# Kernel tuning notes

Measured on AMD Instinct MI355X. Metric: run time of the kernel, lower is better.

Reference implementation:

```python
import jax, jax.numpy as jnp
import numpy as np

WIDTH = 128


def setup_inputs() -> dict:
    key = jax.random.key(0)
    k_logits, k_w1, k_b1, k_w2, k_b2 = jax.random.split(key, 5)
    B, T, V = 32, 256, 4096
    logits = jax.random.normal(k_logits, (B, T, V), dtype=jnp.float32)
    # Linear(1, width): weight [width, 1] -> stored transposed as [1, width]
    w1 = jax.random.normal(k_w1, (1, WIDTH), dtype=jnp.float32) / jnp.sqrt(1.0)
    b1 = jax.random.normal(k_b1, (WIDTH,), dtype=jnp.float32) * 0.1
    # Linear(width, 1): weight [1, width] -> stored transposed as [width, 1]
    w2 = jax.random.normal(k_w2, (WIDTH, 1), dtype=jnp.float32) / jnp.sqrt(WIDTH)
    b2 = jax.random.normal(k_b2, (1,), dtype=jnp.float32) * 0.1
    return {"logits": logits, "w1": w1, "b1": b1, "w2": w2, "b2": b2}


def reference(logits, w1, b1, w2, b2):
    B, T, V = logits.shape
    logits_trim = logits[:, :-1, :]                       # [B, T-1, V]
    # entropy of softmax over the class dim; logits - logsumexp == log_softmax
    logp = jax.nn.log_softmax(logits_trim, axis=-1)       # [B, T-1, V]
    p = jnp.exp(logp)
    entropy = -jnp.sum(p * logp, axis=-1, keepdims=True)  # [B, T-1, 1]
    entropy_max = jnp.log(jnp.asarray(T, dtype=logits.dtype))  # log(num_steps)
    norm = 2.0 * entropy / entropy_max - 1.0              # [B, T-1, 1]
    # tiny 1 -> width -> 1 MLP
    hidden = jax.nn.relu(norm @ w1 + b1)                  # [B, T-1, width]
    lin = (2.0 * hidden) @ w2 + b2                        # [B, T-1, 1]
    # ns = [T-1, T-2, ..., 1]
    ns = jnp.arange(T - 1, 0, -1, dtype=logits.dtype).reshape(1, T - 1, 1)
    flags_trim = jax.nn.sigmoid(lin - jnp.log(ns))        # [B, T-1, 1]
    zeros = jnp.zeros((B, 1, 1), dtype=logits.dtype)
    ones = jnp.ones((B, 1, 1), dtype=logits.dtype)
    flags = jnp.concatenate([zeros, flags_trim, ones], axis=1)  # [B, T+1, 1]
    probabilities = jax.nn.softmax(logits, axis=2)        # [B, T, V]
    residuals = jnp.cumprod(1.0 - flags[:, :-1], axis=1)  # [B, T, 1] survival
    frequencies = probabilities * flags[:, 1:] * residuals  # [B, T, V]
    return frequencies
```

## Files before the change

### kernel.cpp

```cpp
#include <hip/hip_runtime.h>
#include <math.h>

#define T_DIM 256
#define V_DIM 4096
#define WIDTH 128

__device__ __forceinline__ float wave_max(float v) {
#pragma unroll
  for (int o = 32; o > 0; o >>= 1) v = fmaxf(v, __shfl_xor(v, o));
  return v;
}

__device__ __forceinline__ double wave_sum(double v) {
#pragma unroll
  for (int o = 32; o > 0; o >>= 1) v += __shfl_xor(v, o);
  return v;
}

__global__ __launch_bounds__(256) void row_stats(
    const float* __restrict__ logits,
    const float* __restrict__ w1, const float* __restrict__ b1,
    const float* __restrict__ w2, const float* __restrict__ b2,
    float* __restrict__ row_max, double* __restrict__ row_Z,
    double* __restrict__ row_flag) {
  const int row = blockIdx.x;
  const int t = row & (T_DIM - 1);
  const int tid = threadIdx.x;
  const int lane = tid & 63;
  const int wave = tid >> 6;

  const float4* src = (const float4*)(logits + (size_t)row * V_DIM);
  float4 xv[4];
#pragma unroll
  for (int k = 0; k < 4; ++k) xv[k] = src[tid + k * 256];

  float m = -INFINITY;
#pragma unroll
  for (int k = 0; k < 4; ++k)
    m = fmaxf(m, fmaxf(fmaxf(xv[k].x, xv[k].y), fmaxf(xv[k].z, xv[k].w)));
  m = wave_max(m);

  __shared__ float smax[4];
  __shared__ double szs[4], sss[4];
  if (lane == 0) smax[wave] = m;
  __syncthreads();
  m = fmaxf(fmaxf(smax[0], smax[1]), fmaxf(smax[2], smax[3]));

  double z = 0.0, s = 0.0;
#pragma unroll
  for (int k = 0; k < 4; ++k) {
    float vals[4] = {xv[k].x, xv[k].y, xv[k].z, xv[k].w};
#pragma unroll
    for (int j = 0; j < 4; ++j) {
      float sv = vals[j] - m;
      float ev = expf(sv);
      z += (double)ev;
      s += (double)ev * (double)sv;
    }
  }
  z = wave_sum(z);
  s = wave_sum(s);
  if (lane == 0) { szs[wave] = z; sss[wave] = s; }
  __syncthreads();

  if (wave == 0) {
    z = szs[0] + szs[1] + szs[2] + szs[3];
    s = sss[0] + sss[1] + sss[2] + sss[3];
    if (lane == 0) { row_max[row] = m; row_Z[row] = z; }
    if (t < T_DIM - 1) {
      double H = log(z) - s / z;
      double nrm = 2.0 * H / log(256.0) - 1.0;
      double acc = 0.0;
#pragma unroll
      for (int j = lane; j < WIDTH; j += 64) {
        double h = nrm * (double)w1[j] + (double)b1[j];
        h = h > 0.0 ? h : 0.0;
        acc += h * (double)w2[j];
      }
      acc = wave_sum(acc);
      if (lane == 0) {
        double lin = 2.0 * acc + (double)b2[0];
        double xx = lin - log((double)(T_DIM - 1 - t));
        row_flag[row] = 1.0 / (1.0 + exp(-xx));
      }
    }
  }
}

__global__ void cumprod_k(const double* __restrict__ row_Z,
                          const double* __restrict__ row_flag,
                          float* __restrict__ row_scale, int Bn) {
  int b = blockIdx.x * blockDim.x + threadIdx.x;
  if (b >= Bn) return;
  const double* f = row_flag + (size_t)b * T_DIM;
  const double* Z = row_Z + (size_t)b * T_DIM;
  float* sc = row_scale + (size_t)b * T_DIM;
  double r = 1.0;
  for (int t = 0; t < T_DIM; ++t) {
    double ft = (t == 0) ? 0.0 : f[t - 1];
    r *= (1.0 - ft);
    double ftp1 = (t == T_DIM - 1) ? 1.0 : f[t];
    sc[t] = (float)(ftp1 * r / Z[t]);
  }
}

__global__ __launch_bounds__(256) void out_k(const float* __restrict__ logits,
                                             const float* __restrict__ row_max,
                                             const float* __restrict__ row_scale,
                                             float* __restrict__ out) {
  const int row = blockIdx.x;
  const int tid = threadIdx.x;
  const float m = row_max[row];
  const float sc = row_scale[row];
  const float4* src = (const float4*)(logits + (size_t)row * V_DIM);
  float4* dst = (float4*)(out + (size_t)row * V_DIM);
#pragma unroll
  for (int k = 0; k < 4; ++k) {
    float4 x = src[tid + k * 256];
    float4 o;
    o.x = expf(x.x - m) * sc;
    o.y = expf(x.y - m) * sc;
    o.z = expf(x.z - m) * sc;
    o.w = expf(x.w - m) * sc;
    dst[tid + k * 256] = o;
  }
}

extern "C" void kernel_launch(void* const* d_in, const int* in_sizes, int n_in,
                              void* d_out, int out_size, void* d_ws, size_t ws_size,
                              hipStream_t stream) {
  const float* logits = (const float*)d_in[0];
  const float* w1 = (const float*)d_in[1];
  const float* b1 = (const float*)d_in[2];
  const float* w2 = (const float*)d_in[3];
  const float* b2 = (const float*)d_in[4];
  float* out = (float*)d_out;

  const size_t nrows = (size_t)in_sizes[0] / V_DIM;
  const int Bn = (int)(nrows / T_DIM);

  double* row_Z = (double*)d_ws;
  double* row_flag = row_Z + nrows;
  float* row_max = (float*)(row_flag + nrows);
  float* row_scale = row_max + nrows;

  row_stats<<<(int)nrows, 256, 0, stream>>>(logits, w1, b1, w2, b2,
                                            row_max, row_Z, row_flag);
  cumprod_k<<<1, 64, 0, stream>>>(row_Z, row_flag, row_scale, Bn);
  out_k<<<(int)nrows, 256, 0, stream>>>(logits, row_max, row_scale, out);
}
```

Measured before the change: 308.5 us.

## Use float row reductions and parallelize cumprod as per-batch wave scan

Row statistics now accumulate the exp-sum and entropy term in float and use float wave shuffles. Only the four per-wave partials are combined in double, and the tiny MLP runs serially on one lane. The serial single-block cumprod kernel, which used 32 threads each looping over 256 steps, is replaced by one 64-lane block per batch that does a multiplicative shuffle scan. This targets the double-precision arithmetic cost and the latency of the serial scan kernel. In exchange, precision drops slightly in the float accumulation.

```diff
diff --git a/kernel.cpp b/kernel.cpp
--- a/kernel.cpp
+++ b/kernel.cpp
@@ -5,13 +5,19 @@
 #define V_DIM 4096
 #define WIDTH 128
 
-__device__ __forceinline__ float wave_max(float v) {
+__device__ __forceinline__ float wave_max_f(float v) {
 #pragma unroll
   for (int o = 32; o > 0; o >>= 1) v = fmaxf(v, __shfl_xor(v, o));
   return v;
 }
 
-__device__ __forceinline__ double wave_sum(double v) {
+__device__ __forceinline__ float wave_sum_f(float v) {
+#pragma unroll
+  for (int o = 32; o > 0; o >>= 1) v += __shfl_xor(v, o);
+  return v;
+}
+
+__device__ __forceinline__ double wave_sum_d(double v) {
 #pragma unroll
   for (int o = 32; o > 0; o >>= 1) v += __shfl_xor(v, o);
   return v;
@@ -38,15 +44,15 @@
 #pragma unroll
   for (int k = 0; k < 4; ++k)
     m = fmaxf(m, fmaxf(fmaxf(xv[k].x, xv[k].y), fmaxf(xv[k].z, xv[k].w)));
-  m = wave_max(m);
+  m = wave_max_f(m);
 
   __shared__ float smax[4];
-  __shared__ double szs[4], sss[4];
+  __shared__ float szs[4], sss[4];
   if (lane == 0) smax[wave] = m;
   __syncthreads();
   m = fmaxf(fmaxf(smax[0], smax[1]), fmaxf(smax[2], smax[3]));
 
-  double z = 0.0, s = 0.0;
+  float z = 0.f, s = 0.f;
 #pragma unroll
   for (int k = 0; k < 4; ++k) {
     float vals[4] = {xv[k].x, xv[k].y, xv[k].z, xv[k].w};
@@ -54,53 +60,74 @@
     for (int j = 0; j < 4; ++j) {
       float sv = vals[j] - m;
       float ev = expf(sv);
-      z += (double)ev;
-      s += (double)ev * (double)sv;
+      z += ev;
+      s = fmaf(ev, sv, s);
     }
   }
-  z = wave_sum(z);
-  s = wave_sum(s);
+  z = wave_sum_f(z);
+  s = wave_sum_f(s);
   if (lane == 0) { szs[wave] = z; sss[wave] = s; }
   __syncthreads();
 
-  if (wave == 0) {
-    z = szs[0] + szs[1] + szs[2] + szs[3];
-    s = sss[0] + sss[1] + sss[2] + sss[3];
-    if (lane == 0) { row_max[row] = m; row_Z[row] = z; }
+  if (wave == 0 && lane == 0) {
+    double zd = (double)szs[0] + szs[1] + szs[2] + szs[3];
+    double sd = (double)sss[0] + sss[1] + sss[2] + sss[3];
+    row_max[row] = m;
+    row_Z[row] = zd;
     if (t < T_DIM - 1) {
-      double H = log(z) - s / z;
+      double H = log(zd) - sd / zd;
       double nrm = 2.0 * H / log(256.0) - 1.0;
       double acc = 0.0;
-#pragma unroll
-      for (int j = lane; j < WIDTH; j += 64) {
+#pragma unroll 4
+      for (int j = 0; j < WIDTH; ++j) {
         double h = nrm * (double)w1[j] + (double)b1[j];
         h = h > 0.0 ? h : 0.0;
         acc += h * (double)w2[j];
       }
-      acc = wave_sum(acc);
-      if (lane == 0) {
-        double lin = 2.0 * acc + (double)b2[0];
-        double xx = lin - log((double)(T_DIM - 1 - t));
-        row_flag[row] = 1.0 / (1.0 + exp(-xx));
-      }
+      double lin = 2.0 * acc + (double)b2[0];
+      double xx = lin - log((double)(T_DIM - 1 - t));
+      row_flag[row] = 1.0 / (1.0 + exp(-xx));
     }
   }
 }
 
-__global__ void cumprod_k(const double* __restrict__ row_Z,
-                          const double* __restrict__ row_flag,
-                          float* __restrict__ row_scale, int Bn) {
-  int b = blockIdx.x * blockDim.x + threadIdx.x;
-  if (b >= Bn) return;
-  const double* f = row_flag + (size_t)b * T_DIM;
-  const double* Z = row_Z + (size_t)b * T_DIM;
-  float* sc = row_scale + (size_t)b * T_DIM;
-  double r = 1.0;
-  for (int t = 0; t < T_DIM; ++t) {
-    double ft = (t == 0) ? 0.0 : f[t - 1];
-    r *= (1.0 - ft);
-    double ftp1 = (t == T_DIM - 1) ? 1.0 : f[t];
-    sc[t] = (float)(ftp1 * r / Z[t]);
+__global__ __launch_bounds__(64) void cumprod_scan(
+    const double* __restrict__ row_Z, const double* __restrict__ row_flag,
+    float* __restrict__ row_scale) {
+  const int b = blockIdx.x;
+  const int lane = threadIdx.x;
+  __shared__ double fl[T_DIM];
+
+  const double* fb = row_flag + (size_t)b * T_DIM;
+  const double* Zb = row_Z + (size_t)b * T_DIM;
+
+#pragma unroll
+  for (int j = lane; j < T_DIM; j += 64) fl[j] = (j == T_DIM - 1) ? 1.0 : fb[j];
+  __syncthreads();
+
+  double loc[4];
+  double p = 1.0;
+#pragma unroll
+  for (int j = 0; j < 4; ++j) {
+    int t = lane * 4 + j;
+    double flag_t = (t == 0) ? 0.0 : fl[t - 1];
+    p *= (1.0 - flag_t);
+    loc[j] = p;
+  }
+  double inc = p;
+#pragma unroll
+  for (int o = 1; o < 64; o <<= 1) {
+    double up = __shfl_up(inc, o);
+    if (lane >= o) inc *= up;
+  }
+  double exc = __shfl_up(inc, 1);
+  if (lane == 0) exc = 1.0;
+
+#pragma unroll
+  for (int j = 0; j < 4; ++j) {
+    int t = lane * 4 + j;
+    double resid = exc * loc[j];
+    row_scale[(size_t)b * T_DIM + t] = (float)(fl[t] * resid / Zb[t]);
   }
 }
 
@@ -146,6 +173,6 @@
 
   row_stats<<<(int)nrows, 256, 0, stream>>>(logits, w1, b1, w2, b2,
                                             row_max, row_Z, row_flag);
-  cumprod_k<<<1, 64, 0, stream>>>(row_Z, row_flag, row_scale, Bn);
+  cumprod_scan<<<Bn, 64, 0, stream>>>(row_Z, row_flag, row_scale);
   out_k<<<(int)nrows, 256, 0, stream>>>(logits, row_max, row_scale, out);
 }
```

After: 263.5 us. 1.17x faster.
